# Kernel optimization log

Hardware: AMD Instinct MI355X
Metric: run time of the kernel (lower is better)

## Reference

```python
import jax, jax.numpy as jnp
import numpy as np

B, T, E, H = 8, 2048, 1024, 64

def setup_inputs() -> dict:
    key = jax.random.key(0)
    ks = jax.random.split(key, 7)
    s = 1.0 / np.sqrt(E)
    return {
        "x": jax.random.normal(ks[0], (B, T, E), dtype=jnp.float32),
        "Wk": jax.random.normal(ks[1], (E, H), dtype=jnp.float32) * s,
        "bk": jax.random.normal(ks[2], (H,), dtype=jnp.float32) * 0.01,
        "Wq": jax.random.normal(ks[3], (E, H), dtype=jnp.float32) * s,
        "bq": jax.random.normal(ks[4], (H,), dtype=jnp.float32) * 0.01,
        "Wv": jax.random.normal(ks[5], (E, H), dtype=jnp.float32) * s,
        "bv": jax.random.normal(ks[6], (H,), dtype=jnp.float32) * 0.01,
    }

def reference(x, Wk, bk, Wq, bq, Wv, bv):
    # q,k,v: [B, T, H]
    k = x @ Wk + bk
    q = x @ Wq + bq
    v = x @ Wv + bv
    scale = jnp.asarray(H, x.dtype) ** -0.5
    scores = jnp.einsum('bth,bsh->bts', q, k) * scale  # [B, T, T]
    T_ = x.shape[1]
    causal = jnp.tril(jnp.ones((T_, T_), dtype=bool))
    scores = jnp.where(causal, scores, jnp.asarray(-jnp.inf, x.dtype))
    attn = jax.nn.softmax(scores, axis=-1)  # dropout p=0.0 -> identity
    return jnp.einsum('bts,bsh->bth', attn, v)
```

## Files before the change

kernel.cpp:

```cpp
#include <hip/hip_runtime.h>
#include <hip/hip_bf16.h>
#include <math.h>

#define BB 8
#define TT 2048
#define EE 1024
#define HH 64
#define QSCALE 0.18033688011112042f

typedef __attribute__((ext_vector_type(8))) short short8;
typedef __attribute__((ext_vector_type(4))) float f32x4;
typedef __attribute__((ext_vector_type(4))) unsigned short us4;

__device__ inline unsigned short f2bf(float f) {
  union { __hip_bfloat16 h; unsigned short u; } cv;
  cv.h = __float2bfloat16(f);
  return cv.u;
}

__global__ __launch_bounds__(256) void prep_w(
    const float* __restrict__ Wk, const float* __restrict__ Wq,
    const float* __restrict__ Wv, unsigned short* __restrict__ Wf) {
  const int idx = blockIdx.x * 256 + threadIdx.x;
  const int lane = idx & 63, ks = (idx >> 6) & 31, t = idx >> 11;
  const int q = lane & 15, g = lane >> 4;
  const int m = t >> 2, h = (t & 3) * 16 + q;
  const float* W = (m == 0) ? Wk : (m == 1) ? Wq : Wv;
  const float sc = (m == 1) ? QSCALE : 1.f;
  const int e0 = ks * 32 + g * 8;
  unsigned short v[8];
  #pragma unroll
  for (int j = 0; j < 8; ++j) v[j] = f2bf(W[(e0 + j) * 64 + h] * sc);
  *(short8*)&Wf[(size_t)idx * 8] = *(short8*)v;
}

__global__ __launch_bounds__(256) void qkv_proj(
    const float* __restrict__ x,
    const float* __restrict__ bk, const float* __restrict__ bq,
    const float* __restrict__ bv, const unsigned short* __restrict__ Wf,
    unsigned short* __restrict__ kf, unsigned short* __restrict__ qf,
    unsigned short* __restrict__ vf) {
  __shared__ alignas(16) unsigned short xs[16][1040];
  __shared__ alignas(16) unsigned short img[3072];

  const int tid = threadIdx.x;
  const long row0 = (long)blockIdx.x * 16;
  const int w = tid >> 6, lane = tid & 63;
  const int q = lane & 15, g = lane >> 4;

  const float4* xg = (const float4*)&x[row0 * EE];
  #pragma unroll
  for (int i = 0; i < 16; ++i) {
    const int flat = i * 256 + tid;
    const int rr = flat >> 8, c4 = flat & 255;
    const float4 xv = xg[flat];
    us4 pk = {f2bf(xv.x), f2bf(xv.y), f2bf(xv.z), f2bf(xv.w)};
    *(us4*)&xs[rr][c4 * 4] = pk;
  }
  __syncthreads();

  const f32x4 z = {0.f, 0.f, 0.f, 0.f};
  f32x4 acc0 = z, acc1 = z, acc2 = z;
  const unsigned short* wf0 = &Wf[(size_t)w * 16384 + (size_t)lane * 8];

  #pragma unroll 8
  for (int ks = 0; ks < 32; ++ks) {
    const short8 af = *(const short8*)&xs[q][ks * 32 + g * 8];
    const short8 b0 = *(const short8*)&wf0[ks * 512];
    const short8 b1 = *(const short8*)&wf0[65536 + ks * 512];
    const short8 b2 = *(const short8*)&wf0[131072 + ks * 512];
    acc0 = __builtin_amdgcn_mfma_f32_16x16x32_bf16(af, b0, acc0, 0, 0, 0);
    acc1 = __builtin_amdgcn_mfma_f32_16x16x32_bf16(af, b1, acc1, 0, 0, 0);
    acc2 = __builtin_amdgcn_mfma_f32_16x16x32_bf16(af, b2, acc2, 0, 0, 0);
  }

  const int h = w * 16 + q;
  const float biask = bk[h], biasq = bq[h] * QSCALE, biasv = bv[h];
  #pragma unroll
  for (int i = 0; i < 3; ++i) {
    const f32x4 a = (i == 0) ? acc0 : (i == 1) ? acc1 : acc2;
    const float bias = (i == 0) ? biask : (i == 1) ? biasq : biasv;
    #pragma unroll
    for (int r = 0; r < 4; ++r) {
      const int tlh = 4 * g + r;
      const unsigned short ov = f2bf(a[r] + bias);
      if (i == 2) {
        img[2048 + w * 256 + (tlh >> 3) * 128 + q * 8 + (tlh & 7)] = ov;
      } else {
        const int g2 = (w & 1) * 2 + (q >> 3);
        img[i * 1024 + (w >> 1) * 512 + g2 * 128 + tlh * 8 + (q & 7)] = ov;
      }
    }
  }
  __syncthreads();

  const long bidx = row0 >> 11;
  const int tlg = (int)(row0 & 2047);
  const size_t tb16 = (size_t)bidx * 131072 + (size_t)(tlg >> 4) * 1024;
  const size_t vb32 = (size_t)bidx * 131072 + (size_t)(tlg >> 5) * 2048;
  const int ks0v = (tlg >> 4) & 1;
  if (tid < 128) {
    *(short8*)&kf[tb16 + (size_t)tid * 8] = *(const short8*)&img[tid * 8];
    const int wv = tid >> 5, uu = (tid >> 4) & 1, qv = tid & 15;
    *(short8*)&vf[vb32 + wv * 512 + (2 * ks0v + uu) * 128 + qv * 8] =
        *(const short8*)&img[2048 + tid * 8];
  } else if (tid < 256) {
    const int t2 = tid - 128;
    *(short8*)&qf[tb16 + (size_t)t2 * 8] = *(const short8*)&img[1024 + t2 * 8];
  }
}

#define BODY(KC0, KC1, KC2, KC3, KN0, KN1, KN2, KN3, tt, PREF) do {          \
    const unsigned short* vp_ = vfb + (size_t)(tt) * 2048;                   \
    const short8 V0 = *(const short8*)&vp_[0];                               \
    const short8 V1 = *(const short8*)&vp_[512];                             \
    const short8 V2 = *(const short8*)&vp_[1024];                            \
    const short8 V3 = *(const short8*)&vp_[1536];                            \
    if (PREF) {                                                              \
      const unsigned short* kp_ = kfb + (size_t)((tt) + stride) * 2048;      \
      KN0 = *(const short8*)&kp_[0];                                         \
      KN1 = *(const short8*)&kp_[512];                                       \
      KN2 = *(const short8*)&kp_[1024];                                      \
      KN3 = *(const short8*)&kp_[1536];                                      \
    }                                                                        \
    f32x4 sa = __builtin_amdgcn_mfma_f32_16x16x32_bf16(KC0, Qf0, z, 0,0,0);  \
    sa = __builtin_amdgcn_mfma_f32_16x16x32_bf16(KC1, Qf1, sa, 0,0,0);       \
    f32x4 sb = __builtin_amdgcn_mfma_f32_16x16x32_bf16(KC2, Qf0, z, 0,0,0);  \
    sb = __builtin_amdgcn_mfma_f32_16x16x32_bf16(KC3, Qf1, sb, 0,0,0);       \
    const int k0_ = (tt) * 32;                                               \
    if (k0_ + 31 > q0) {                                                     \
      _Pragma("unroll")                                                      \
      for (int r = 0; r < 4; ++r) {                                          \
        if (k0_ + 4 * g + r > qg) sa[r] = -INFINITY;                         \
        if (k0_ + 16 + 4 * g + r > qg) sb[r] = -INFINITY;                    \
      }                                                                      \
    }                                                                        \
    float pmax = fmaxf(fmaxf(fmaxf(sa[0], sa[1]), fmaxf(sa[2], sa[3])),      \
                       fmaxf(fmaxf(sb[0], sb[1]), fmaxf(sb[2], sb[3])));     \
    if (!__all(pmax <= m + 8.0f)) {                                          \
      float tmax = pmax;                                                     \
      tmax = fmaxf(tmax, __shfl_xor(tmax, 16));                              \
      tmax = fmaxf(tmax, __shfl_xor(tmax, 32));                              \
      const float nm = fmaxf(m, tmax);                                       \
      const float rs = __builtin_amdgcn_exp2f(m - nm);                       \
      l *= rs; o0 *= rs; o1 *= rs; o2 *= rs; o3 *= rs;                       \
      m = nm;                                                                \
    }                                                                        \
    float ps = 0.f;                                                          \
    _Pragma("unroll")                                                        \
    for (int r = 0; r < 4; ++r) {                                            \
      sa[r] = __builtin_amdgcn_exp2f(sa[r] - m); ps += sa[r];                \
      sb[r] = __builtin_amdgcn_exp2f(sb[r] - m); ps += sb[r];                \
    }                                                                        \
    l += ps;                                                                 \
    unsigned pw0, pw1, pw2, pw3;                                             \
    asm("v_cvt_pk_bf16_f32 %0, %1, %2" : "=v"(pw0) : "v"(sa[0]), "v"(sa[1]));\
    asm("v_cvt_pk_bf16_f32 %0, %1, %2" : "=v"(pw1) : "v"(sa[2]), "v"(sa[3]));\
    asm("v_cvt_pk_bf16_f32 %0, %1, %2" : "=v"(pw2) : "v"(sb[0]), "v"(sb[1]));\
    asm("v_cvt_pk_bf16_f32 %0, %1, %2" : "=v"(pw3) : "v"(sb[2]), "v"(sb[3]));\
    const int srcA = q + ((g & 1) << 5);                                     \
    const int srcB = srcA + 16;                                              \
    const unsigned r0a = __shfl((int)pw0, srcA);                             \
    const unsigned r1a = __shfl((int)pw1, srcA);                             \
    const unsigned r2a = __shfl((int)pw2, srcA);                             \
    const unsigned r3a = __shfl((int)pw3, srcA);                             \
    const unsigned r0b = __shfl((int)pw0, srcB);                             \
    const unsigned r1b = __shfl((int)pw1, srcB);                             \
    const unsigned r2b = __shfl((int)pw2, srcB);                             \
    const unsigned r3b = __shfl((int)pw3, srcB);                             \
    union { unsigned u[4]; short8 s; } pf_;                                  \
    const bool hi_ = (g >= 2);                                               \
    pf_.u[0] = hi_ ? r2a : r0a;                                              \
    pf_.u[1] = hi_ ? r3a : r1a;                                              \
    pf_.u[2] = hi_ ? r2b : r0b;                                              \
    pf_.u[3] = hi_ ? r3b : r1b;                                              \
    const short8 Pf = pf_.s;                                                 \
    o0 = __builtin_amdgcn_mfma_f32_16x16x32_bf16(V0, Pf, o0, 0,0,0);         \
    o1 = __builtin_amdgcn_mfma_f32_16x16x32_bf16(V1, Pf, o1, 0,0,0);         \
    o2 = __builtin_amdgcn_mfma_f32_16x16x32_bf16(V2, Pf, o2, 0,0,0);         \
    o3 = __builtin_amdgcn_mfma_f32_16x16x32_bf16(V3, Pf, o3, 0,0,0);         \
  } while (0)

__global__ __launch_bounds__(512) void attn_fwd(
    const unsigned short* __restrict__ qf, const unsigned short* __restrict__ kf,
    const unsigned short* __restrict__ vf, float* __restrict__ out) {
  __shared__ float accS[8][64][17];
  __shared__ float mlS[8][2][16];

  const int tid = threadIdx.x;
  const int w = tid >> 6, lane = tid & 63;
  const int q = lane & 15, g = lane >> 4;

  const int b = blockIdx.x & 7;
  const int p = blockIdx.x >> 3;
  const int s1 = 127 - p;
  const int nt0 = (p + 2) >> 1, nt1 = (129 - p) >> 1;
  int k = (8 * nt0 + 32) / 65;
  if (k < 1) k = 1;
  if (k > 7) k = 7;

  const bool onS0 = (w < k);
  const int s = onS0 ? p : s1;
  const int nt = onS0 ? nt0 : nt1;
  const int stride = onS0 ? k : (8 - k);
  int t = onS0 ? w : (w - k);

  const int q0 = s * 16;
  const int qg = q0 + q;

  const unsigned short* kfb = kf + (size_t)b * 131072 + (size_t)lane * 8;
  const unsigned short* vfb = vf + (size_t)b * 131072 + (size_t)lane * 8;
  const unsigned short* qfb = qf + (size_t)b * 131072 + (size_t)s * 1024 +
                              (size_t)lane * 8;
  const short8 Qf0 = *(const short8*)&qfb[0];
  const short8 Qf1 = *(const short8*)&qfb[512];

  const f32x4 z = {0.f, 0.f, 0.f, 0.f};
  float m = -3.0e38f, l = 0.f;
  f32x4 o0 = z, o1 = z, o2 = z, o3 = z;

  {
    short8 A0, A1, A2, A3, B0, B1, B2, B3;
    const unsigned short* kp0 = kfb + (size_t)t * 2048;
    A0 = *(const short8*)&kp0[0];
    A1 = *(const short8*)&kp0[512];
    A2 = *(const short8*)&kp0[1024];
    A3 = *(const short8*)&kp0[1536];
    for (;;) {
      bool pf = (t + stride) < nt;
      BODY(A0, A1, A2, A3, B0, B1, B2, B3, t, pf);
      if (!pf) break;
      t += stride;
      pf = (t + stride) < nt;
      BODY(B0, B1, B2, B3, A0, A1, A2, A3, t, pf);
      if (!pf) break;
      t += stride;
    }
  }

  float lq = l;
  lq += __shfl_xor(lq, 16);
  lq += __shfl_xor(lq, 32);
  #pragma unroll
  for (int hb = 0; hb < 4; ++hb) {
    const f32x4 a = (hb == 0) ? o0 : (hb == 1) ? o1 : (hb == 2) ? o2 : o3;
    #pragma unroll
    for (int r = 0; r < 4; ++r) accS[w][16 * hb + 4 * g + r][q] = a[r];
  }
  if (g == 0) { mlS[w][0][q] = m; mlS[w][1][q] = lq; }
  __syncthreads();

  const int half = tid >> 8;
  const int sm = half ? s1 : p;
  const int lo = half ? k : 0, hi = half ? 8 : k;
  const int row = tid & 63, qq = (tid >> 6) & 3;
  const long obase = ((long)b * TT + sm * 16) * 64;
  #pragma unroll
  for (int kk = 0; kk < 4; ++kk) {
    const int qv = qq + 4 * kk;
    float M = -INFINITY;
    for (int i = lo; i < hi; ++i) M = fmaxf(M, mlS[i][0][qv]);
    float L = 0.f, acc = 0.f;
    for (int i = lo; i < hi; ++i) {
      const float fi = __builtin_amdgcn_exp2f(mlS[i][0][qv] - M);
      L += fi * mlS[i][1][qv];
      acc += fi * accS[i][row][qv];
    }
    out[obase + (long)qv * 64 + row] = acc / L;
  }
}

extern "C" void kernel_launch(void* const* d_in, const int* in_sizes, int n_in,
                              void* d_out, int out_size, void* d_ws, size_t ws_size,
                              hipStream_t stream) {
  const float* x  = (const float*)d_in[0];
  const float* Wk = (const float*)d_in[1];
  const float* bk = (const float*)d_in[2];
  const float* Wq = (const float*)d_in[3];
  const float* bq = (const float*)d_in[4];
  const float* Wv = (const float*)d_in[5];
  const float* bv = (const float*)d_in[6];
  float* out = (float*)d_out;

  unsigned short* qfb = (unsigned short*)d_ws;
  unsigned short* kfb = qfb + (size_t)1048576;
  unsigned short* vfb = kfb + (size_t)1048576;
  unsigned short* Wf  = vfb + (size_t)1048576;

  prep_w<<<dim3(96), 256, 0, stream>>>(Wk, Wq, Wv, Wf);
  qkv_proj<<<dim3(1024), 256, 0, stream>>>(x, bk, bq, bv, Wf, kfb, qfb, vfb);
  attn_fwd<<<dim3(512), 512, 0, stream>>>(qfb, kfb, vfb, out);
}
```

Baseline: 49.70 us.

## Tile QKV projection over 64 rows per block to reuse weight fragments

Each qkv_proj block now covers 64 rows instead of 16, and each wave computes 3 of the 12 output column tiles across 4 row subtiles. Every weight fragment loaded from global memory is therefore reused for 4 MFMAs, and weight loads are double-buffered two k-steps ahead. The x loads are batched 16 float4 at a time to raise memory-level parallelism. The grid drops to 256 blocks and shared memory grows to about 156KB, so each CU holds at most one block. That risks underfilling the GPU's CUs and hiding less latency.

```diff
diff --git a/kernel.cpp b/kernel.cpp
--- a/kernel.cpp
+++ b/kernel.cpp
@@ -34,61 +34,120 @@
   *(short8*)&Wf[(size_t)idx * 8] = *(short8*)v;
 }
 
-__global__ __launch_bounds__(256) void qkv_proj(
+__global__ __launch_bounds__(256, 1) void qkv_proj(
     const float* __restrict__ x,
     const float* __restrict__ bk, const float* __restrict__ bq,
     const float* __restrict__ bv, const unsigned short* __restrict__ Wf,
     unsigned short* __restrict__ kf, unsigned short* __restrict__ qf,
     unsigned short* __restrict__ vf) {
-  __shared__ alignas(16) unsigned short xs[16][1040];
-  __shared__ alignas(16) unsigned short img[3072];
+  __shared__ alignas(16) unsigned short xs[64][1032];
+  __shared__ alignas(16) unsigned short img[12288];
 
   const int tid = threadIdx.x;
-  const long row0 = (long)blockIdx.x * 16;
+  const long row0 = (long)blockIdx.x * 64;
   const int w = tid >> 6, lane = tid & 63;
   const int q = lane & 15, g = lane >> 4;
 
   const float4* xg = (const float4*)&x[row0 * EE];
-  #pragma unroll
-  for (int i = 0; i < 16; ++i) {
-    const int flat = i * 256 + tid;
-    const int rr = flat >> 8, c4 = flat & 255;
-    const float4 xv = xg[flat];
-    us4 pk = {f2bf(xv.x), f2bf(xv.y), f2bf(xv.z), f2bf(xv.w)};
-    *(us4*)&xs[rr][c4 * 4] = pk;
+  #pragma unroll 1
+  for (int sw = 0; sw < 4; ++sw) {
+    float4 st[16];
+    #pragma unroll
+    for (int i = 0; i < 16; ++i) st[i] = xg[sw * 4096 + i * 256 + tid];
+    #pragma unroll
+    for (int i = 0; i < 16; ++i) {
+      const int flat = sw * 4096 + i * 256 + tid;
+      const int rr = flat >> 8, c4 = flat & 255;
+      us4 pk = {f2bf(st[i].x), f2bf(st[i].y), f2bf(st[i].z), f2bf(st[i].w)};
+      *(us4*)&xs[rr][c4 * 4] = pk;
+    }
   }
   __syncthreads();
 
   const f32x4 z = {0.f, 0.f, 0.f, 0.f};
-  f32x4 acc0 = z, acc1 = z, acc2 = z;
-  const unsigned short* wf0 = &Wf[(size_t)w * 16384 + (size_t)lane * 8];
-
-  #pragma unroll 8
+  f32x4 acc[3][4];
+  #pragma unroll
+  for (int i = 0; i < 3; ++i)
+    #pragma unroll
+    for (int st = 0; st < 4; ++st) acc[i][st] = z;
+
+  const unsigned short* wf0 = &Wf[(size_t)(3 * w) * 16384 + (size_t)lane * 8];
+
+  short8 b0A, b1A, b2A, b0B, b1B, b2B;
+  b0A = *(const short8*)&wf0[0];
+  b1A = *(const short8*)&wf0[16384];
+  b2A = *(const short8*)&wf0[32768];
+  b0B = *(const short8*)&wf0[512];
+  b1B = *(const short8*)&wf0[16384 + 512];
+  b2B = *(const short8*)&wf0[32768 + 512];
+
+  #pragma unroll
   for (int ks = 0; ks < 32; ++ks) {
-    const short8 af = *(const short8*)&xs[q][ks * 32 + g * 8];
-    const short8 b0 = *(const short8*)&wf0[ks * 512];
-    const short8 b1 = *(const short8*)&wf0[65536 + ks * 512];
-    const short8 b2 = *(const short8*)&wf0[131072 + ks * 512];
-    acc0 = __builtin_amdgcn_mfma_f32_16x16x32_bf16(af, b0, acc0, 0, 0, 0);
-    acc1 = __builtin_amdgcn_mfma_f32_16x16x32_bf16(af, b1, acc1, 0, 0, 0);
-    acc2 = __builtin_amdgcn_mfma_f32_16x16x32_bf16(af, b2, acc2, 0, 0, 0);
-  }
-
-  const int h = w * 16 + q;
-  const float biask = bk[h], biasq = bq[h] * QSCALE, biasv = bv[h];
+    const short8 a0 = *(const short8*)&xs[q][ks * 32 + g * 8];
+    const short8 a1 = *(const short8*)&xs[16 + q][ks * 32 + g * 8];
+    const short8 a2 = *(const short8*)&xs[32 + q][ks * 32 + g * 8];
+    const short8 a3 = *(const short8*)&xs[48 + q][ks * 32 + g * 8];
+    if ((ks & 1) == 0) {
+      acc[0][0] = __builtin_amdgcn_mfma_f32_16x16x32_bf16(a0, b0A, acc[0][0], 0, 0, 0);
+      acc[0][1] = __builtin_amdgcn_mfma_f32_16x16x32_bf16(a1, b0A, acc[0][1], 0, 0, 0);
+      acc[0][2] = __builtin_amdgcn_mfma_f32_16x16x32_bf16(a2, b0A, acc[0][2], 0, 0, 0);
+      acc[0][3] = __builtin_amdgcn_mfma_f32_16x16x32_bf16(a3, b0A, acc[0][3], 0, 0, 0);
+      acc[1][0] = __builtin_amdgcn_mfma_f32_16x16x32_bf16(a0, b1A, acc[1][0], 0, 0, 0);
+      acc[1][1] = __builtin_amdgcn_mfma_f32_16x16x32_bf16(a1, b1A, acc[1][1], 0, 0, 0);
+      acc[1][2] = __builtin_amdgcn_mfma_f32_16x16x32_bf16(a2, b1A, acc[1][2], 0, 0, 0);
+      acc[1][3] = __builtin_amdgcn_mfma_f32_16x16x32_bf16(a3, b1A, acc[1][3], 0, 0, 0);
+      acc[2][0] = __builtin_amdgcn_mfma_f32_16x16x32_bf16(a0, b2A, acc[2][0], 0, 0, 0);
+      acc[2][1] = __builtin_amdgcn_mfma_f32_16x16x32_bf16(a1, b2A, acc[2][1], 0, 0, 0);
+      acc[2][2] = __builtin_amdgcn_mfma_f32_16x16x32_bf16(a2, b2A, acc[2][2], 0, 0, 0);
+      acc[2][3] = __builtin_amdgcn_mfma_f32_16x16x32_bf16(a3, b2A, acc[2][3], 0, 0, 0);
+      if (ks + 2 < 32) {
+        b0A = *(const short8*)&wf0[(ks + 2) * 512];
+        b1A = *(const short8*)&wf0[16384 + (ks + 2) * 512];
+        b2A = *(const short8*)&wf0[32768 + (ks + 2) * 512];
+      }
+    } else {
+      acc[0][0] = __builtin_amdgcn_mfma_f32_16x16x32_bf16(a0, b0B, acc[0][0], 0, 0, 0);
+      acc[0][1] = __builtin_amdgcn_mfma_f32_16x16x32_bf16(a1, b0B, acc[0][1], 0, 0, 0);
+      acc[0][2] = __builtin_amdgcn_mfma_f32_16x16x32_bf16(a2, b0B, acc[0][2], 0, 0, 0);
+      acc[0][3] = __builtin_amdgcn_mfma_f32_16x16x32_bf16(a3, b0B, acc[0][3], 0, 0, 0);
+      acc[1][0] = __builtin_amdgcn_mfma_f32_16x16x32_bf16(a0, b1B, acc[1][0], 0, 0, 0);
+      acc[1][1] = __builtin_amdgcn_mfma_f32_16x16x32_bf16(a1, b1B, acc[1][1], 0, 0, 0);
+      acc[1][2] = __builtin_amdgcn_mfma_f32_16x16x32_bf16(a2, b1B, acc[1][2], 0, 0, 0);
+      acc[1][3] = __builtin_amdgcn_mfma_f32_16x16x32_bf16(a3, b1B, acc[1][3], 0, 0, 0);
+      acc[2][0] = __builtin_amdgcn_mfma_f32_16x16x32_bf16(a0, b2B, acc[2][0], 0, 0, 0);
+      acc[2][1] = __builtin_amdgcn_mfma_f32_16x16x32_bf16(a1, b2B, acc[2][1], 0, 0, 0);
+      acc[2][2] = __builtin_amdgcn_mfma_f32_16x16x32_bf16(a2, b2B, acc[2][2], 0, 0, 0);
+      acc[2][3] = __builtin_amdgcn_mfma_f32_16x16x32_bf16(a3, b2B, acc[2][3], 0, 0, 0);
+      if (ks + 2 < 32) {
+        b0B = *(const short8*)&wf0[(ks + 2) * 512];
+        b1B = *(const short8*)&wf0[16384 + (ks + 2) * 512];
+        b2B = *(const short8*)&wf0[32768 + (ks + 2) * 512];
+      }
+    }
+  }
+
   #pragma unroll
   for (int i = 0; i < 3; ++i) {
-    const f32x4 a = (i == 0) ? acc0 : (i == 1) ? acc1 : acc2;
-    const float bias = (i == 0) ? biask : (i == 1) ? biasq : biasv;
-    #pragma unroll
-    for (int r = 0; r < 4; ++r) {
-      const int tlh = 4 * g + r;
-      const unsigned short ov = f2bf(a[r] + bias);
-      if (i == 2) {
-        img[2048 + w * 256 + (tlh >> 3) * 128 + q * 8 + (tlh & 7)] = ov;
-      } else {
-        const int g2 = (w & 1) * 2 + (q >> 3);
-        img[i * 1024 + (w >> 1) * 512 + g2 * 128 + tlh * 8 + (q & 7)] = ov;
+    const int tgl = 3 * w + i;
+    const int mm = tgl >> 2, hb = tgl & 3;
+    const int h = hb * 16 + q;
+    const float bias = (mm == 0) ? bk[h] : (mm == 1) ? bq[h] * QSCALE : bv[h];
+    #pragma unroll
+    for (int st = 0; st < 4; ++st) {
+      const f32x4 a = acc[i][st];
+      #pragma unroll
+      for (int r = 0; r < 4; ++r) {
+        const int tlh = 4 * g + r;
+        const unsigned short ov = f2bf(a[r] + bias);
+        if (mm == 2) {
+          const int tl5 = (st & 1) * 16 + tlh;
+          img[8192 + (st >> 1) * 2048 + hb * 512 + (tl5 >> 3) * 128 + q * 8 +
+              (tl5 & 7)] = ov;
+        } else {
+          const int g2 = (h & 31) >> 3;
+          img[mm * 4096 + st * 1024 + (h >> 5) * 512 + g2 * 128 + tlh * 8 +
+              (h & 7)] = ov;
+        }
       }
     }
   }
@@ -96,17 +155,14 @@
 
   const long bidx = row0 >> 11;
   const int tlg = (int)(row0 & 2047);
-  const size_t tb16 = (size_t)bidx * 131072 + (size_t)(tlg >> 4) * 1024;
-  const size_t vb32 = (size_t)bidx * 131072 + (size_t)(tlg >> 5) * 2048;
-  const int ks0v = (tlg >> 4) & 1;
-  if (tid < 128) {
-    *(short8*)&kf[tb16 + (size_t)tid * 8] = *(const short8*)&img[tid * 8];
-    const int wv = tid >> 5, uu = (tid >> 4) & 1, qv = tid & 15;
-    *(short8*)&vf[vb32 + wv * 512 + (2 * ks0v + uu) * 128 + qv * 8] =
-        *(const short8*)&img[2048 + tid * 8];
-  } else if (tid < 256) {
-    const int t2 = tid - 128;
-    *(short8*)&qf[tb16 + (size_t)t2 * 8] = *(const short8*)&img[1024 + t2 * 8];
+  const size_t b16 = (size_t)bidx * 131072 + (size_t)(tlg >> 4) * 1024;
+  const size_t b32 = (size_t)bidx * 131072 + (size_t)(tlg >> 5) * 2048;
+  #pragma unroll
+  for (int j = 0; j < 2; ++j) {
+    const int t2 = tid + 256 * j;
+    *(short8*)&kf[b16 + (size_t)t2 * 8] = *(const short8*)&img[t2 * 8];
+    *(short8*)&qf[b16 + (size_t)t2 * 8] = *(const short8*)&img[4096 + t2 * 8];
+    *(short8*)&vf[b32 + (size_t)t2 * 8] = *(const short8*)&img[8192 + t2 * 8];
   }
 }
 
@@ -288,6 +344,6 @@
   unsigned short* Wf  = vfb + (size_t)1048576;
 
   prep_w<<<dim3(96), 256, 0, stream>>>(Wk, Wq, Wv, Wf);
-  qkv_proj<<<dim3(1024), 256, 0, stream>>>(x, bk, bq, bv, Wf, kfb, qfb, vfb);
+  qkv_proj<<<dim3(256), 256, 0, stream>>>(x, bk, bq, bv, Wf, kfb, qfb, vfb);
   attn_fwd<<<dim3(512), 512, 0, stream>>>(qfb, kfb, vfb, out);
 }
```

After: 52.62 us. +5.9%, slower.
